# Kernel tuning notes

Measured on AMD Instinct MI355X. Metric: run time of the kernel, lower is better.

## Reference

```python
import jax, jax.numpy as jnp
import numpy as np

# Config mirroring init_kwargs
B, N, DM = 16, 512, 512          # batch, max_ast_len, hidden_size
PAR_HEADS, BRO_HEADS = 4, 4
H = PAR_HEADS + BRO_HEADS        # 8 heads
DK = DM // H                     # 64
R = 8                            # max_rel_pos
L = 2                            # num_layers
DFF = 4 * DM
EPS = 1e-5


def setup_inputs() -> dict:
    key = jax.random.key(0)
    ks = jax.random.split(key, 24)
    s = 0.02
    inp = {
        "src_emb": jax.random.normal(ks[0], (B, N, DM), jnp.float32),
        "par_edges": jax.random.randint(ks[1], (B, R, N), 0, N, jnp.int32),
        "bro_edges": jax.random.randint(ks[2], (B, R, N), 0, N, jnp.int32),
        # relative-position embedding tables (par heads ++ bro heads along head axis,
        # exactly what concat_vec(rel_par_*, rel_bro_*, dim=1) produces): [H, R, DK]
        "rel_q": s * jax.random.normal(ks[3], (H, R, DK), jnp.float32),
        "rel_k": s * jax.random.normal(ks[4], (H, R, DK), jnp.float32),
        "rel_v": s * jax.random.normal(ks[5], (H, R, DK), jnp.float32),
        # per-layer weights, stacked over layers
        "Wq": s * jax.random.normal(ks[6], (L, DM, DM), jnp.float32),
        "Wk": s * jax.random.normal(ks[7], (L, DM, DM), jnp.float32),
        "Wv": s * jax.random.normal(ks[8], (L, DM, DM), jnp.float32),
        "Wo": s * jax.random.normal(ks[9], (L, DM, DM), jnp.float32),
        "ln1_g": jnp.ones((L, DM), jnp.float32),
        "ln1_b": jnp.zeros((L, DM), jnp.float32),
        "W1": s * jax.random.normal(ks[10], (L, DM, DFF), jnp.float32),
        "b1": jnp.zeros((L, DFF), jnp.float32),
        "W2": s * jax.random.normal(ks[11], (L, DFF, DM), jnp.float32),
        "b2": jnp.zeros((L, DM), jnp.float32),
        "ln2_g": jnp.ones((L, DM), jnp.float32),
        "ln2_b": jnp.zeros((L, DM), jnp.float32),
        "normf_g": jnp.ones((DM,), jnp.float32),
        "normf_b": jnp.zeros((DM,), jnp.float32),
    }
    return inp


def _ln(x, g, b):
    m = x.mean(-1, keepdims=True)
    v = ((x - m) ** 2).mean(-1, keepdims=True)
    return (x - m) * jax.lax.rsqrt(v + EPS) * g + b


def _gather_nodes(t, idx):
    # t: [B,H,N,DK], idx: [B,H,R,N,1] -> [B,H,R,N,DK] gathered along node axis
    t_b = jnp.broadcast_to(t[:, :, None], (B, H, R, N, DK))
    return jnp.take_along_axis(t_b, idx, axis=3)


def _forward(src_emb, rel_q, rel_k, rel_v, Wq, Wk, Wv, Wo, ln1_g, ln1_b,
             W1, b1, W2, b2, ln2_g, ln2_b, normf_g, normf_b,
             par_edges, bro_edges):
    # start_nodes = concat_pos: repeat par edges over par heads, bro over bro heads
    start = jnp.concatenate(
        [jnp.repeat(par_edges[:, None], PAR_HEADS, axis=1),
         jnp.repeat(bro_edges[:, None], BRO_HEADS, axis=1)], axis=1)  # [B,H,R,N]
    idx = start[..., None].astype(jnp.int32)  # [B,H,R,N,1]
    scale = 1.0 / np.sqrt(DK)
    x = src_emb
    for i in range(L):
        q = (x @ Wq[i]).reshape(B, N, H, DK).transpose(0, 2, 1, 3)  # bhnd
        k = (x @ Wk[i]).reshape(B, N, H, DK).transpose(0, 2, 1, 3)
        v = (x @ Wv[i]).reshape(B, N, H, DK).transpose(0, 2, 1, 3)
        k_s = _gather_nodes(k, idx)  # [B,H,R,N,DK]
        v_s = _gather_nodes(v, idx)
        # Shaw-style relational scores over the R sparse neighbors only
        scores = (jnp.einsum('bhnd,bhrnd->bhrn', q, k_s)
                  + jnp.einsum('bhnd,hrd->bhrn', q, rel_k)
                  + jnp.einsum('hrd,bhrnd->bhrn', rel_q, k_s)) * scale
        attn = jax.nn.softmax(scores, axis=2)  # softmax over relative positions
        ctx = (jnp.einsum('bhrn,bhrnd->bhnd', attn, v_s)
               + jnp.einsum('bhrn,hrd->bhnd', attn, rel_v))
        ctx = ctx.transpose(0, 2, 1, 3).reshape(B, N, DM)
        x = _ln(x + ctx @ Wo[i], ln1_g[i], ln1_b[i])
        ff = jax.nn.relu(x @ W1[i] + b1[i]) @ W2[i] + b2[i]
        x = _ln(x + ff, ln2_g[i], ln2_b[i])
    return _ln(x, normf_g, normf_b)  # final self.norm


def reference(src_emb, par_edges, bro_edges, rel_q, rel_k, rel_v,
              Wq, Wk, Wv, Wo, ln1_g, ln1_b, W1, b1, W2, b2,
              ln2_g, ln2_b, normf_g, normf_b):
    return _forward(src_emb, rel_q, rel_k, rel_v, Wq, Wk, Wv, Wo,
                    ln1_g, ln1_b, W1, b1, W2, b2, ln2_g, ln2_b,
                    normf_g, normf_b, par_edges, bro_edges)
```

## Files before the change

### kernel.cpp

```cpp
#include <hip/hip_runtime.h>
#include <hip/hip_bf16.h>


#define BB 16
#define NN 512
#define DMM 512
#define HH 8
#define DKK 64
#define RR 8
#define LL 2
#define DFFV 2048
#define PAR_HEADS 4
#define EPSV 1e-5f

typedef __bf16 bf16x8 __attribute__((ext_vector_type(8)));
typedef float f32x4 __attribute__((ext_vector_type(4)));
typedef unsigned short u16x8 __attribute__((ext_vector_type(8)));

__device__ __forceinline__ unsigned short f2bf(float f) {
    unsigned u = __float_as_uint(f);
    u += 0x7fff + ((u >> 16) & 1);
    return (unsigned short)(u >> 16);
}
__device__ __forceinline__ float bf2f(unsigned short u) {
    return __uint_as_float(((unsigned)u) << 16);
}

__global__ __launch_bounds__(256) void transpose_qkvo_kernel(
    const float* __restrict__ Wq, const float* __restrict__ Wk,
    const float* __restrict__ Wv, const float* __restrict__ Wo,
    unsigned short* __restrict__ wqkvT, unsigned short* __restrict__ woT)
{
    __shared__ float tile[32][33];
    int layer = blockIdx.z >> 2, which = blockIdx.z & 3;
    const float* s = (which == 0 ? Wq : which == 1 ? Wk : which == 2 ? Wv : Wo)
                     + (size_t)layer * DMM * DMM;
    unsigned short* d = (which < 3)
        ? wqkvT + (size_t)layer * 1536 * DMM + (size_t)which * DMM * DMM
        : woT + (size_t)layer * DMM * DMM;
    int k0 = blockIdx.y * 32, n0 = blockIdx.x * 32;
    int tx = threadIdx.x & 31, ty = threadIdx.x >> 5;
#pragma unroll
    for (int i = 0; i < 4; ++i)
        tile[ty + i * 8][tx] = s[(size_t)(k0 + ty + i * 8) * DMM + (n0 + tx)];
    __syncthreads();
#pragma unroll
    for (int i = 0; i < 4; ++i)
        d[(size_t)(n0 + ty + i * 8) * DMM + (k0 + tx)] = f2bf(tile[tx][ty + i * 8]);
}

__global__ __launch_bounds__(256) void transpose_w_kernel(
    const float* __restrict__ src, unsigned short* __restrict__ dst,
    int K, int N, size_t zStride)
{
    __shared__ float tile[32][33];
    const float* s = src + (size_t)blockIdx.z * K * N;
    unsigned short* d = dst + (size_t)blockIdx.z * zStride;
    int k0 = blockIdx.y * 32, n0 = blockIdx.x * 32;
    int tx = threadIdx.x & 31, ty = threadIdx.x >> 5;
#pragma unroll
    for (int i = 0; i < 4; ++i)
        tile[ty + i * 8][tx] = s[(size_t)(k0 + ty + i * 8) * N + (n0 + tx)];
    __syncthreads();
#pragma unroll
    for (int i = 0; i < 4; ++i)
        d[(size_t)(n0 + ty + i * 8) * K + (k0 + tx)] = f2bf(tile[tx][ty + i * 8]);
}

__global__ __launch_bounds__(256) void convert_x_kernel(
    const float* __restrict__ src, float* __restrict__ x, unsigned short* __restrict__ xb, int n4)
{
    int i = blockIdx.x * blockDim.x + threadIdx.x;
    int stride = gridDim.x * blockDim.x;
    for (; i < n4; i += stride) {
        float4 f = ((const float4*)src)[i];
        ((float4*)x)[i] = f;
        ushort4 u;
        u.x = f2bf(f.x); u.y = f2bf(f.y); u.z = f2bf(f.z); u.w = f2bf(f.w);
        ((ushort4*)xb)[i] = u;
    }
}

template<bool OUTBF, bool DORELU>
__global__ __launch_bounds__(256) void gemm_kernel(
    const unsigned short* __restrict__ A,
    const unsigned short* __restrict__ Bt,
    float* __restrict__ Cf,
    unsigned short* __restrict__ Cb,
    const float* __restrict__ bias,
    int M, int N, int K, int kLen)
{
    constexpr int BM = 128, BN = 64, BK = 64;
    __shared__ __align__(16) unsigned short As[BM * BK];
    __shared__ __align__(16) unsigned short Bs[BN * BK];
    int tid = threadIdx.x, lane = tid & 63, w = tid >> 6;
    int wr = w >> 1, wc = w & 1;

    int gx = gridDim.x;
    int nwg = gx * gridDim.y;
    int flat = blockIdx.x + gx * blockIdx.y;
    int qq = nwg >> 3;
    int swz = (flat & 7) * qq + (flat >> 3);
    int bx = swz % gx, by = swz / gx;
    int mBase = by * BM, nBase = bx * BN;
    int kStart = blockIdx.z * kLen;

    f32x4 acc[4][2];
#pragma unroll
    for (int i = 0; i < 4; ++i)
#pragma unroll
        for (int j = 0; j < 2; ++j) acc[i][j] = (f32x4){0.f, 0.f, 0.f, 0.f};

    for (int k0 = kStart; k0 < kStart + kLen; k0 += BK) {
#pragma unroll
        for (int it = 0; it < 4; ++it) {
            int i = it * 256 + tid;
            int row = i >> 3, slot = i & 7;
            int gcol = (slot ^ (row & 7)) * 8;
            const unsigned short* ga = A + (size_t)(mBase + row) * K + k0 + gcol;
            __builtin_amdgcn_global_load_lds(
                (const __attribute__((address_space(1))) void*)ga,
                (__attribute__((address_space(3))) void*)(As + i * 8), 16, 0, 0);
        }
#pragma unroll
        for (int it = 0; it < 2; ++it) {
            int i = it * 256 + tid;
            int row = i >> 3, slot = i & 7;
            int gcol = (slot ^ (row & 7)) * 8;
            const unsigned short* gb = Bt + (size_t)(nBase + row) * K + k0 + gcol;
            __builtin_amdgcn_global_load_lds(
                (const __attribute__((address_space(1))) void*)gb,
                (__attribute__((address_space(3))) void*)(Bs + i * 8), 16, 0, 0);
        }
        __syncthreads();

        int rsel = lane & 15, g0 = lane >> 4;
        bf16x8 a[4][2], b[2][2];
#pragma unroll
        for (int m = 0; m < 4; ++m) {
            int row = wr * 64 + m * 16 + rsel;
#pragma unroll
            for (int ks = 0; ks < 2; ++ks) {
                int s = (g0 + ks * 4) ^ (row & 7);
                a[m][ks] = *(const bf16x8*)((const char*)As + row * 128 + s * 16);
            }
        }
#pragma unroll
        for (int n = 0; n < 2; ++n) {
            int row = wc * 32 + n * 16 + rsel;
#pragma unroll
            for (int ks = 0; ks < 2; ++ks) {
                int s = (g0 + ks * 4) ^ (row & 7);
                b[n][ks] = *(const bf16x8*)((const char*)Bs + row * 128 + s * 16);
            }
        }
#pragma unroll
        for (int m = 0; m < 4; ++m)
#pragma unroll
            for (int n = 0; n < 2; ++n)
#pragma unroll
                for (int ks = 0; ks < 2; ++ks)
                    acc[m][n] = __builtin_amdgcn_mfma_f32_16x16x32_bf16(a[m][ks], b[n][ks], acc[m][n], 0, 0, 0);
        __syncthreads();
    }

    size_t zoff = (size_t)blockIdx.z * M * N;
    int rbase = (lane >> 4) * 4;
    int cloc = lane & 15;
#pragma unroll
    for (int m = 0; m < 4; ++m) {
#pragma unroll
        for (int n = 0; n < 2; ++n) {
            int col = nBase + wc * 32 + n * 16 + cloc;
            float bv = bias ? bias[col] : 0.0f;
#pragma unroll
            for (int j = 0; j < 4; ++j) {
                int row = mBase + wr * 64 + m * 16 + rbase + j;
                float val = acc[m][n][j] + bv;
                if (DORELU) val = fmaxf(val, 0.0f);
                if (OUTBF) Cb[zoff + (size_t)row * N + col] = f2bf(val);
                else       Cf[zoff + (size_t)row * N + col] = val;
            }
        }
    }
}

__global__ __launch_bounds__(256) void attn_kernel(
    const unsigned short* __restrict__ qkv,
    const int* __restrict__ par, const int* __restrict__ bro,
    const float* __restrict__ relq, const float* __restrict__ relk,
    const float* __restrict__ relv, unsigned short* __restrict__ cb)
{
    int f = blockIdx.x;
    int xcd = f & 7;
    int j = f >> 3;
    int b = xcd + 8 * (j & 1);
    int rem = j >> 1;
    int h = rem >> 4;
    int n0 = (rem & 15) * 32;
    int w = threadIdx.x >> 6;
    int lane = threadIdx.x & 63;
    int nw = n0 + w * 8;

    float rq[RR], rk[RR], rv[RR];
#pragma unroll
    for (int r = 0; r < RR; ++r) {
        rq[r] = relq[(h * RR + r) * DKK + lane];
        rk[r] = relk[(h * RR + r) * DKK + lane];
        rv[r] = relv[(h * RR + r) * DKK + lane];
    }
    const int* edges = (h < PAR_HEADS) ? par : bro;
    int e_all = edges[(b * RR + (lane & 7)) * NN + nw + (lane >> 3)];

    const unsigned short* qrow = qkv + (size_t)b * NN * 1536 + h * DKK;

#pragma unroll
    for (int nl = 0; nl < 8; ++nl) {
        int n = nw + nl;
        float qd = bf2f(qrow[(size_t)n * 1536 + lane]);
        float t[RR];
        int e[RR];
#pragma unroll
        for (int r = 0; r < RR; ++r) {
            int er = __builtin_amdgcn_readlane(e_all, nl * 8 + r);
            e[r] = er;
            float kd = bf2f(qkv[(size_t)(b * NN + er) * 1536 + DMM + h * DKK + lane]);
            t[r] = kd * (qd + rq[r]) + qd * rk[r];
        }
        {
            bool hb = lane & 4;
#pragma unroll
            for (int rr = 0; rr < 4; ++rr) {
                float send = hb ? t[rr] : t[rr + 4];
                float keep = hb ? t[rr + 4] : t[rr];
                t[rr] = keep + __shfl_xor(send, 4, 64);
            }
        }
        {
            bool hb = lane & 2;
#pragma unroll
            for (int rr = 0; rr < 2; ++rr) {
                float send = hb ? t[rr] : t[rr + 2];
                float keep = hb ? t[rr + 2] : t[rr];
                t[rr] = keep + __shfl_xor(send, 2, 64);
            }
        }
        {
            bool hb = lane & 1;
            float send = hb ? t[0] : t[1];
            float keep = hb ? t[1] : t[0];
            t[0] = keep + __shfl_xor(send, 1, 64);
        }
        float s = t[0];
        s += __shfl_xor(s, 8, 64);
        s += __shfl_xor(s, 16, 64);
        s += __shfl_xor(s, 32, 64);
        s *= 0.125f;
        float mx = s;
        mx = fmaxf(mx, __shfl_xor(mx, 1, 64));
        mx = fmaxf(mx, __shfl_xor(mx, 2, 64));
        mx = fmaxf(mx, __shfl_xor(mx, 4, 64));
        float ee = __expf(s - mx);
        float den = ee;
        den += __shfl_xor(den, 1, 64);
        den += __shfl_xor(den, 2, 64);
        den += __shfl_xor(den, 4, 64);
        float a = ee / den;
        float od = 0.f;
#pragma unroll
        for (int r = 0; r < RR; ++r) {
            float ar = __shfl(a, (lane & 56) | r, 64);
            float vd = bf2f(qkv[(size_t)(b * NN + e[r]) * 1536 + 2 * DMM + h * DKK + lane]);
            od = fmaf(ar, vd + rv[r], od);
        }
        cb[(size_t)(b * NN + n) * DMM + h * DKK + lane] = f2bf(od);
    }
}

__global__ __launch_bounds__(256) void ln_kernel(
    const float* __restrict__ xin, const float* __restrict__ add0,
    const float* __restrict__ add1, const float* __restrict__ bias,
    float* __restrict__ xout, unsigned short* __restrict__ xbout,
    const float* __restrict__ g, const float* __restrict__ bb)
{
    int row = blockIdx.x * 4 + (threadIdx.x >> 6);
    int lane = threadIdx.x & 63;
    int c0 = lane * 8;
    const float* xr = xin + (size_t)row * DMM + c0;
    float vals[8];
    {
        float4 v0 = *(const float4*)xr;
        float4 v1 = *(const float4*)(xr + 4);
        vals[0] = v0.x; vals[1] = v0.y; vals[2] = v0.z; vals[3] = v0.w;
        vals[4] = v1.x; vals[5] = v1.y; vals[6] = v1.z; vals[7] = v1.w;
    }
    if (add0) {
        const float* ar = add0 + (size_t)row * DMM + c0;
        float4 v0 = *(const float4*)ar, v1 = *(const float4*)(ar + 4);
        vals[0] += v0.x; vals[1] += v0.y; vals[2] += v0.z; vals[3] += v0.w;
        vals[4] += v1.x; vals[5] += v1.y; vals[6] += v1.z; vals[7] += v1.w;
    }
    if (add1) {
        const float* ar = add1 + (size_t)row * DMM + c0;
        float4 v0 = *(const float4*)ar, v1 = *(const float4*)(ar + 4);
        vals[0] += v0.x; vals[1] += v0.y; vals[2] += v0.z; vals[3] += v0.w;
        vals[4] += v1.x; vals[5] += v1.y; vals[6] += v1.z; vals[7] += v1.w;
    }
    if (bias) {
        float4 v0 = *(const float4*)(bias + c0), v1 = *(const float4*)(bias + c0 + 4);
        vals[0] += v0.x; vals[1] += v0.y; vals[2] += v0.z; vals[3] += v0.w;
        vals[4] += v1.x; vals[5] += v1.y; vals[6] += v1.z; vals[7] += v1.w;
    }
    float s = 0.f;
#pragma unroll
    for (int j = 0; j < 8; ++j) s += vals[j];
#pragma unroll
    for (int off = 32; off > 0; off >>= 1) s += __shfl_xor(s, off, 64);
    float mean = s * (1.0f / DMM);
    float s2 = 0.f;
#pragma unroll
    for (int j = 0; j < 8; ++j) { float d = vals[j] - mean; s2 += d * d; }
#pragma unroll
    for (int off = 32; off > 0; off >>= 1) s2 += __shfl_xor(s2, off, 64);
    float inv = rsqrtf(s2 * (1.0f / DMM) + EPSV);

    float4 gv0 = *(const float4*)(g + c0), gv1 = *(const float4*)(g + c0 + 4);
    float4 bv0 = *(const float4*)(bb + c0), bv1 = *(const float4*)(bb + c0 + 4);
    float y[8];
    y[0] = (vals[0] - mean) * inv * gv0.x + bv0.x;
    y[1] = (vals[1] - mean) * inv * gv0.y + bv0.y;
    y[2] = (vals[2] - mean) * inv * gv0.z + bv0.z;
    y[3] = (vals[3] - mean) * inv * gv0.w + bv0.w;
    y[4] = (vals[4] - mean) * inv * gv1.x + bv1.x;
    y[5] = (vals[5] - mean) * inv * gv1.y + bv1.y;
    y[6] = (vals[6] - mean) * inv * gv1.z + bv1.z;
    y[7] = (vals[7] - mean) * inv * gv1.w + bv1.w;

    float* xo = xout + (size_t)row * DMM + c0;
    *(float4*)xo = make_float4(y[0], y[1], y[2], y[3]);
    *(float4*)(xo + 4) = make_float4(y[4], y[5], y[6], y[7]);
    if (xbout) {
        u16x8 u;
#pragma unroll
        for (int j = 0; j < 8; ++j) u[j] = f2bf(y[j]);
        *(u16x8*)(xbout + (size_t)row * DMM + c0) = u;
    }
}

extern "C" void kernel_launch(void* const* d_in, const int* in_sizes, int n_in,
                              void* d_out, int out_size, void* d_ws, size_t ws_size,
                              hipStream_t stream)
{
    const float* src_emb = (const float*)d_in[0];
    const int*   par     = (const int*)d_in[1];
    const int*   bro     = (const int*)d_in[2];
    const float* rel_q   = (const float*)d_in[3];
    const float* rel_k   = (const float*)d_in[4];
    const float* rel_v   = (const float*)d_in[5];
    const float* Wq      = (const float*)d_in[6];
    const float* Wk      = (const float*)d_in[7];
    const float* Wv      = (const float*)d_in[8];
    const float* Wo      = (const float*)d_in[9];
    const float* ln1_g   = (const float*)d_in[10];
    const float* ln1_b   = (const float*)d_in[11];
    const float* W1      = (const float*)d_in[12];
    const float* b1      = (const float*)d_in[13];
    const float* W2      = (const float*)d_in[14];
    const float* b2      = (const float*)d_in[15];
    const float* ln2_g   = (const float*)d_in[16];
    const float* ln2_b   = (const float*)d_in[17];
    const float* normf_g = (const float*)d_in[18];
    const float* normf_b = (const float*)d_in[19];

    const size_t MB = 1024 * 1024;
    const int M = BB * NN;
    char* ws = (char*)d_ws;
    float*          p    = (float*)(ws + 0 * MB);
    unsigned short* qkvb = (unsigned short*)(ws + 0 * MB);
    unsigned short* h1   = (unsigned short*)(ws + 32 * MB);
    unsigned short* xb   = (unsigned short*)(ws + 64 * MB);
    unsigned short* cbuf = (unsigned short*)(ws + 72 * MB);
    unsigned short* wqkvT = (unsigned short*)(ws + 80 * MB);
    unsigned short* woT  = wqkvT + (size_t)LL * 1536 * DMM;
    unsigned short* w1T  = woT + (size_t)LL * DMM * DMM;
    unsigned short* w2T  = w1T + (size_t)LL * DMM * DFFV;
    float* p0 = p;
    float* p1 = p + (size_t)M * DMM;
    float* x = (float*)d_out;

    transpose_qkvo_kernel<<<dim3(16, 16, LL * 4), 256, 0, stream>>>(
        Wq, Wk, Wv, Wo, wqkvT, woT);
    transpose_w_kernel<<<dim3(DFFV / 32, DMM / 32, LL), 256, 0, stream>>>(
        W1, w1T, DMM, DFFV, (size_t)DMM * DFFV);
    transpose_w_kernel<<<dim3(DMM / 32, DFFV / 32, LL), 256, 0, stream>>>(
        W2, w2T, DFFV, DMM, (size_t)DMM * DFFV);

    convert_x_kernel<<<2048, 256, 0, stream>>>(src_emb, x, xb, M * DMM / 4);

    for (int l = 0; l < LL; ++l) {
        const unsigned short* wqkv_l = wqkvT + (size_t)l * 1536 * DMM;
        const unsigned short* wo_l = woT + (size_t)l * DMM * DMM;
        const unsigned short* w1_l = w1T + (size_t)l * DMM * DFFV;
        const unsigned short* w2_l = w2T + (size_t)l * DFFV * DMM;

        gemm_kernel<true, false><<<dim3(1536 / 64, M / 128, 1), 256, 0, stream>>>(
            xb, wqkv_l, nullptr, qkvb, nullptr, M, 1536, DMM, DMM);

        attn_kernel<<<2048, 256, 0, stream>>>(qkvb, par, bro, rel_q, rel_k, rel_v, cbuf);

        gemm_kernel<false, false><<<dim3(512 / 64, M / 128, 2), 256, 0, stream>>>(
            cbuf, wo_l, p, nullptr, nullptr, M, DMM, DMM, DMM / 2);
        ln_kernel<<<M / 4, 256, 0, stream>>>(x, p0, p1, nullptr, x, xb,
                                             ln1_g + l * DMM, ln1_b + l * DMM);

        gemm_kernel<true, true><<<dim3(DFFV / 64, M / 128, 1), 256, 0, stream>>>(
            xb, w1_l, nullptr, h1, b1 + l * DFFV, M, DFFV, DMM, DMM);
        gemm_kernel<false, false><<<dim3(512 / 64, M / 128, 2), 256, 0, stream>>>(
            h1, w2_l, p, nullptr, nullptr, M, DMM, DFFV, DFFV / 2);
        ln_kernel<<<M / 4, 256, 0, stream>>>(x, p0, p1, b2 + l * DMM, x, xb,
                                             ln2_g + l * DMM, ln2_b + l * DMM);
    }

    ln_kernel<<<M / 4, 256, 0, stream>>>(x, nullptr, nullptr, nullptr, x, nullptr,
                                         normf_g, normf_b);
}
```

Before: 457.2 us.

## Keep residual stream in bf16 only and widen QKV/FFN1 GEMM tiles

```diff
diff --git a/kernel.cpp b/kernel.cpp
--- a/kernel.cpp
+++ b/kernel.cpp
@@ -68,20 +68,19 @@
 }
 
 __global__ __launch_bounds__(256) void convert_x_kernel(
-    const float* __restrict__ src, float* __restrict__ x, unsigned short* __restrict__ xb, int n4)
+    const float* __restrict__ src, unsigned short* __restrict__ xb, int n4)
 {
     int i = blockIdx.x * blockDim.x + threadIdx.x;
     int stride = gridDim.x * blockDim.x;
     for (; i < n4; i += stride) {
         float4 f = ((const float4*)src)[i];
-        ((float4*)x)[i] = f;
         ushort4 u;
         u.x = f2bf(f.x); u.y = f2bf(f.y); u.z = f2bf(f.z); u.w = f2bf(f.w);
         ((ushort4*)xb)[i] = u;
     }
 }
 
-template<bool OUTBF, bool DORELU>
+template<int BM, int BN, bool OUTBF, bool DORELU>
 __global__ __launch_bounds__(256) void gemm_kernel(
     const unsigned short* __restrict__ A,
     const unsigned short* __restrict__ Bt,
@@ -90,7 +89,9 @@
     const float* __restrict__ bias,
     int M, int N, int K, int kLen)
 {
-    constexpr int BM = 128, BN = 64, BK = 64;
+    constexpr int BK = 64;
+    constexpr int MT = BM / 32;
+    constexpr int NT = BN / 32;
     __shared__ __align__(16) unsigned short As[BM * BK];
     __shared__ __align__(16) unsigned short Bs[BN * BK];
     int tid = threadIdx.x, lane = tid & 63, w = tid >> 6;
@@ -105,15 +106,15 @@
     int mBase = by * BM, nBase = bx * BN;
     int kStart = blockIdx.z * kLen;
 
-    f32x4 acc[4][2];
-#pragma unroll
-    for (int i = 0; i < 4; ++i)
-#pragma unroll
-        for (int j = 0; j < 2; ++j) acc[i][j] = (f32x4){0.f, 0.f, 0.f, 0.f};
+    f32x4 acc[MT][NT];
+#pragma unroll
+    for (int i = 0; i < MT; ++i)
+#pragma unroll
+        for (int j = 0; j < NT; ++j) acc[i][j] = (f32x4){0.f, 0.f, 0.f, 0.f};
 
     for (int k0 = kStart; k0 < kStart + kLen; k0 += BK) {
 #pragma unroll
-        for (int it = 0; it < 4; ++it) {
+        for (int it = 0; it < BM * 8 / 256; ++it) {
             int i = it * 256 + tid;
             int row = i >> 3, slot = i & 7;
             int gcol = (slot ^ (row & 7)) * 8;
@@ -123,7 +124,7 @@
                 (__attribute__((address_space(3))) void*)(As + i * 8), 16, 0, 0);
         }
 #pragma unroll
-        for (int it = 0; it < 2; ++it) {
+        for (int it = 0; it < BN * 8 / 256; ++it) {
             int i = it * 256 + tid;
             int row = i >> 3, slot = i & 7;
             int gcol = (slot ^ (row & 7)) * 8;
@@ -135,10 +136,10 @@
         __syncthreads();
 
         int rsel = lane & 15, g0 = lane >> 4;
-        bf16x8 a[4][2], b[2][2];
-#pragma unroll
-        for (int m = 0; m < 4; ++m) {
-            int row = wr * 64 + m * 16 + rsel;
+        bf16x8 a[MT][2], b[NT][2];
+#pragma unroll
+        for (int m = 0; m < MT; ++m) {
+            int row = wr * (BM / 2) + m * 16 + rsel;
 #pragma unroll
             for (int ks = 0; ks < 2; ++ks) {
                 int s = (g0 + ks * 4) ^ (row & 7);
@@ -146,8 +147,8 @@
             }
         }
 #pragma unroll
-        for (int n = 0; n < 2; ++n) {
-            int row = wc * 32 + n * 16 + rsel;
+        for (int n = 0; n < NT; ++n) {
+            int row = wc * (BN / 2) + n * 16 + rsel;
 #pragma unroll
             for (int ks = 0; ks < 2; ++ks) {
                 int s = (g0 + ks * 4) ^ (row & 7);
@@ -155,9 +156,9 @@
             }
         }
 #pragma unroll
-        for (int m = 0; m < 4; ++m)
-#pragma unroll
-            for (int n = 0; n < 2; ++n)
+        for (int m = 0; m < MT; ++m)
+#pragma unroll
+            for (int n = 0; n < NT; ++n)
 #pragma unroll
                 for (int ks = 0; ks < 2; ++ks)
                     acc[m][n] = __builtin_amdgcn_mfma_f32_16x16x32_bf16(a[m][ks], b[n][ks], acc[m][n], 0, 0, 0);
@@ -168,14 +169,14 @@
     int rbase = (lane >> 4) * 4;
     int cloc = lane & 15;
 #pragma unroll
-    for (int m = 0; m < 4; ++m) {
-#pragma unroll
-        for (int n = 0; n < 2; ++n) {
-            int col = nBase + wc * 32 + n * 16 + cloc;
+    for (int m = 0; m < MT; ++m) {
+#pragma unroll
+        for (int n = 0; n < NT; ++n) {
+            int col = nBase + wc * (BN / 2) + n * 16 + cloc;
             float bv = bias ? bias[col] : 0.0f;
 #pragma unroll
             for (int j = 0; j < 4; ++j) {
-                int row = mBase + wr * 64 + m * 16 + rbase + j;
+                int row = mBase + wr * (BM / 2) + m * 16 + rbase + j;
                 float val = acc[m][n][j] + bv;
                 if (DORELU) val = fmaxf(val, 0.0f);
                 if (OUTBF) Cb[zoff + (size_t)row * N + col] = f2bf(val);
@@ -278,21 +279,19 @@
 }
 
 __global__ __launch_bounds__(256) void ln_kernel(
-    const float* __restrict__ xin, const float* __restrict__ add0,
+    const unsigned short* __restrict__ xbin, const float* __restrict__ add0,
     const float* __restrict__ add1, const float* __restrict__ bias,
-    float* __restrict__ xout, unsigned short* __restrict__ xbout,
+    unsigned short* __restrict__ xbout, float* __restrict__ xfout,
     const float* __restrict__ g, const float* __restrict__ bb)
 {
     int row = blockIdx.x * 4 + (threadIdx.x >> 6);
     int lane = threadIdx.x & 63;
     int c0 = lane * 8;
-    const float* xr = xin + (size_t)row * DMM + c0;
     float vals[8];
     {
-        float4 v0 = *(const float4*)xr;
-        float4 v1 = *(const float4*)(xr + 4);
-        vals[0] = v0.x; vals[1] = v0.y; vals[2] = v0.z; vals[3] = v0.w;
-        vals[4] = v1.x; vals[5] = v1.y; vals[6] = v1.z; vals[7] = v1.w;
+        u16x8 u = *(const u16x8*)(xbin + (size_t)row * DMM + c0);
+#pragma unroll
+        for (int j = 0; j < 8; ++j) vals[j] = bf2f(u[j]);
     }
     if (add0) {
         const float* ar = add0 + (size_t)row * DMM + c0;
@@ -336,14 +335,16 @@
     y[6] = (vals[6] - mean) * inv * gv1.z + bv1.z;
     y[7] = (vals[7] - mean) * inv * gv1.w + bv1.w;
 
-    float* xo = xout + (size_t)row * DMM + c0;
-    *(float4*)xo = make_float4(y[0], y[1], y[2], y[3]);
-    *(float4*)(xo + 4) = make_float4(y[4], y[5], y[6], y[7]);
     if (xbout) {
         u16x8 u;
 #pragma unroll
         for (int j = 0; j < 8; ++j) u[j] = f2bf(y[j]);
         *(u16x8*)(xbout + (size_t)row * DMM + c0) = u;
+    }
+    if (xfout) {
+        float* xo = xfout + (size_t)row * DMM + c0;
+        *(float4*)xo = make_float4(y[0], y[1], y[2], y[3]);
+        *(float4*)(xo + 4) = make_float4(y[4], y[5], y[6], y[7]);
     }
 }
 
@@ -395,7 +396,7 @@
     transpose_w_kernel<<<dim3(DMM / 32, DFFV / 32, LL), 256, 0, stream>>>(
         W2, w2T, DFFV, DMM, (size_t)DMM * DFFV);
 
-    convert_x_kernel<<<2048, 256, 0, stream>>>(src_emb, x, xb, M * DMM / 4);
+    convert_x_kernel<<<2048, 256, 0, stream>>>(src_emb, xb, M * DMM / 4);
 
     for (int l = 0; l < LL; ++l) {
         const unsigned short* wqkv_l = wqkvT + (size_t)l * 1536 * DMM;
@@ -403,24 +404,24 @@
         const unsigned short* w1_l = w1T + (size_t)l * DMM * DFFV;
         const unsigned short* w2_l = w2T + (size_t)l * DFFV * DMM;
 
-        gemm_kernel<true, false><<<dim3(1536 / 64, M / 128, 1), 256, 0, stream>>>(
+        gemm_kernel<128, 128, true, false><<<dim3(1536 / 128, M / 128, 1), 256, 0, stream>>>(
             xb, wqkv_l, nullptr, qkvb, nullptr, M, 1536, DMM, DMM);
 
         attn_kernel<<<2048, 256, 0, stream>>>(qkvb, par, bro, rel_q, rel_k, rel_v, cbuf);
 
-        gemm_kernel<false, false><<<dim3(512 / 64, M / 128, 2), 256, 0, stream>>>(
+        gemm_kernel<128, 64, false, false><<<dim3(512 / 64, M / 128, 2), 256, 0, stream>>>(
             cbuf, wo_l, p, nullptr, nullptr, M, DMM, DMM, DMM / 2);
-        ln_kernel<<<M / 4, 256, 0, stream>>>(x, p0, p1, nullptr, x, xb,
+        ln_kernel<<<M / 4, 256, 0, stream>>>(xb, p0, p1, nullptr, xb, nullptr,
                                              ln1_g + l * DMM, ln1_b + l * DMM);
 
-        gemm_kernel<true, true><<<dim3(DFFV / 64, M / 128, 1), 256, 0, stream>>>(
+        gemm_kernel<128, 128, true, true><<<dim3(DFFV / 128, M / 128, 1), 256, 0, stream>>>(
             xb, w1_l, nullptr, h1, b1 + l * DFFV, M, DFFV, DMM, DMM);
-        gemm_kernel<false, false><<<dim3(512 / 64, M / 128, 2), 256, 0, stream>>>(
+        gemm_kernel<128, 64, false, false><<<dim3(512 / 64, M / 128, 2), 256, 0, stream>>>(
             h1, w2_l, p, nullptr, nullptr, M, DMM, DFFV, DFFV / 2);
-        ln_kernel<<<M / 4, 256, 0, stream>>>(x, p0, p1, b2 + l * DMM, x, xb,
+        ln_kernel<<<M / 4, 256, 0, stream>>>(xb, p0, p1, b2 + l * DMM, xb, nullptr,
                                              ln2_g + l * DMM, ln2_b + l * DMM);
     }
 
-    ln_kernel<<<M / 4, 256, 0, stream>>>(x, nullptr, nullptr, nullptr, x, nullptr,
+    ln_kernel<<<M / 4, 256, 0, stream>>>(xb, nullptr, nullptr, nullptr, nullptr, x,
                                          normf_g, normf_b);
 }
```

New measurement: 438.0 us. 1.04x faster.
